# Performance work log

Measured on AMD Instinct MI355X. Metric: run time of the kernel, lower is better.

## Reference

```python
import jax, jax.numpy as jnp
import numpy as np

F, N, D, K = 32, 4096, 64, 512
COMMITMENT_COST = 0.25


def setup_inputs() -> dict:
    key = jax.random.key(0)
    k1, k2 = jax.random.split(key)
    inputs = jax.random.normal(k1, (F, N, D), dtype=jnp.float32)
    # GlorotUniform on weight shape [F, D, K]
    limit = float(np.sqrt(6.0 / (D + K)))
    w = jax.random.uniform(k2, (F, D, K), dtype=jnp.float32, minval=-limit, maxval=limit)
    return {"inputs": inputs, "w": w}


def reference(inputs, w):
    # inputs: [F, N, D], w: [F, D, K]
    distances = (
        jnp.sum(inputs ** 2, axis=2, keepdims=True)
        - 2.0 * jnp.einsum('fnd,fdk->fnk', inputs, w)
        + jnp.sum(w ** 2, axis=1, keepdims=True)
    )
    enc_idx = jnp.argmin(distances, axis=2)  # [F, N]
    w_t = jnp.swapaxes(w, 1, 2)  # [F, K, D]
    quantized = jnp.take_along_axis(w_t, enc_idx[:, :, None], axis=1)  # [F, N, D]
    e_latent_loss = jnp.mean((jax.lax.stop_gradient(quantized) - inputs) ** 2)
    q_latent_loss = jnp.mean((quantized - jax.lax.stop_gradient(inputs)) ** 2)
    loss = q_latent_loss + COMMITMENT_COST * e_latent_loss
    # straight-through estimator
    output = inputs + jax.lax.stop_gradient(quantized - inputs)
    return output, loss
```

## Files before the change

### kernel.cpp

```cpp
#include <hip/hip_runtime.h>
#include <math.h>

#define NF 32
#define NN 4096
#define ND 64
#define NK 512

#define LOSS_SCALE (1.25f / (float)(NF * NN * ND))
#define RESCUE_TAU 5.5e-4f

typedef short bf16x8 __attribute__((ext_vector_type(8)));
typedef float f32x4 __attribute__((ext_vector_type(4)));

static __device__ __forceinline__ unsigned short f2bf_rne(float f) {
    unsigned int u = __float_as_uint(f);
    u += 0x7FFFu + ((u >> 16) & 1u);
    return (unsigned short)(u >> 16);
}
static __device__ __forceinline__ float bf2f(unsigned short h) {
    return __uint_as_float(((unsigned int)h) << 16);
}

static __device__ __forceinline__ void gload_lds16(const void* g, void* l) {
    __builtin_amdgcn_global_load_lds(
        (const __attribute__((address_space(1))) unsigned int*)g,
        (__attribute__((address_space(3))) unsigned int*)l, 16, 0, 0);
}

__global__ __launch_bounds__(256)
void vq_prep_w(const float* __restrict__ w, float* __restrict__ wt,
               unsigned short* __restrict__ wh, unsigned short* __restrict__ wl,
               float* __restrict__ w2h, float* __restrict__ loss_slot) {
    __shared__ float lds[64 * 65];
    const int t  = threadIdx.x;
    const int f  = blockIdx.x >> 3;
    const int k0 = (blockIdx.x & 7) * 64;
    const float* __restrict__ wf = w + (size_t)f * ND * NK;

    if (blockIdx.x == 0 && t == 0) *loss_slot = 0.0f;

    {
        const int d = t >> 2, qq = t & 3;
#pragma unroll
        for (int i = 0; i < 4; ++i) {
            const int c4 = qq + i * 4;
            const float4 v = *(const float4*)(wf + (size_t)d * NK + k0 + c4 * 4);
            lds[d * 65 + c4 * 4 + 0] = v.x;
            lds[d * 65 + c4 * 4 + 1] = v.y;
            lds[d * 65 + c4 * 4 + 2] = v.z;
            lds[d * 65 + c4 * 4 + 3] = v.w;
        }
    }
    __syncthreads();

    const int k = t >> 2, p = t & 3;
    float v[16];
    float s = 0.0f;
#pragma unroll
    for (int j = 0; j < 16; ++j) {
        v[j] = lds[(p * 16 + j) * 65 + k];
        s = fmaf(v[j], v[j], s);
    }
    s += __shfl_xor(s, 1, 64);
    s += __shfl_xor(s, 2, 64);
    if (p == 0) w2h[f * NK + k0 + k] = 0.5f * s;

    const size_t rowo = ((size_t)f * NK + k0 + k) * ND + p * 16;
    unsigned short hh[16], ll[16];
#pragma unroll
    for (int j = 0; j < 16; ++j) {
        hh[j] = f2bf_rne(v[j]);
        ll[j] = f2bf_rne(v[j] - bf2f(hh[j]));
    }
#pragma unroll
    for (int i = 0; i < 4; ++i) {
        *(float4*)(wt + rowo + i * 4) =
            make_float4(v[i*4+0], v[i*4+1], v[i*4+2], v[i*4+3]);
        *(ushort4*)(wh + rowo + i * 4) =
            make_ushort4(hh[i*4+0], hh[i*4+1], hh[i*4+2], hh[i*4+3]);
        *(ushort4*)(wl + rowo + i * 4) =
            make_ushort4(ll[i*4+0], ll[i*4+1], ll[i*4+2], ll[i*4+3]);
    }
}

__global__ __launch_bounds__(256, 4)
void vq_argmin(const float* __restrict__ x_in,
               const unsigned short* __restrict__ wh,
               const unsigned short* __restrict__ wl,
               const float* __restrict__ wt,
               const float* __restrict__ w2h,
               float* __restrict__ out,
               float* __restrict__ loss_slot) {
    const int b    = blockIdx.x;
    const int j    = b >> 3;
    const int f    = (b & 7) * 4 + (j & 3);
    const int xt   = j >> 2;
    const int tid  = threadIdx.x;
    const int wave = tid >> 6;
    const int lane = tid & 63;
    const int lc   = lane & 15;
    const int q    = lane >> 4;
    const int n0   = xt * 128 + wave * 32;
    const int g0b  = f * NN + xt * 128;

    __shared__ float w2s[NK];
    __shared__ __align__(16) unsigned short bstage[2][8192];
    __shared__ unsigned int lds_key[128];
    __shared__ unsigned char lds_flag[128];
    __shared__ float wsum[4];

    for (int t = tid; t < NK; t += 256) w2s[t] = w2h[f * NK + t];

    bf16x8 ah[2][2], al[2][2];
    const float* __restrict__ xbase = x_in + ((size_t)f * NN + n0 + lc) * ND;
#pragma unroll
    for (int mt = 0; mt < 2; ++mt) {
#pragma unroll
        for (int s = 0; s < 2; ++s) {
            const float* p = xbase + mt * 16 * ND + s * 32 + q * 8;
            float4 u0 = *(const float4*)(p);
            float4 u1 = *(const float4*)(p + 4);
            float xv[8] = {-u0.x, -u0.y, -u0.z, -u0.w, -u1.x, -u1.y, -u1.z, -u1.w};
            bf16x8 hh, ll;
#pragma unroll
            for (int jj = 0; jj < 8; ++jj) {
                unsigned short hb = f2bf_rne(xv[jj]);
                unsigned short lb = f2bf_rne(xv[jj] - bf2f(hb));
                hh[jj] = (short)hb;
                ll[jj] = (short)lb;
            }
            ah[mt][s] = hh;
            al[mt][s] = ll;
        }
    }

    const unsigned short* __restrict__ whf = wh + (size_t)f * NK * ND;
    const unsigned short* __restrict__ wlf = wl + (size_t)f * NK * ND;

    float k1[8], k2[8];
#pragma unroll
    for (int ri = 0; ri < 8; ++ri) { k1[ri] = INFINITY; k2[ri] = INFINITY; }

#define STAGE(st, pb) do {                                                  \
    _Pragma("unroll")                                                       \
    for (int rep = 0; rep < 4; ++rep) {                                     \
        const int c  = wave * 4 + rep;                                      \
        const int tl = c >> 2;                                              \
        const int sg = (c >> 1) & 1;                                        \
        const unsigned short* src = ((c & 1) ? wlf : whf) +                 \
            (size_t)((st) * 64 + tl * 16 + lc) * ND + q * 8 + sg * 32;      \
        gload_lds16(src, &bstage[pb][c * 512]);                             \
    }                                                                       \
} while (0)

    STAGE(0, 0);

    for (int st = 0; st < 8; ++st) {
        __syncthreads();
        if (st < 7) STAGE(st + 1, (st + 1) & 1);
        const unsigned short* __restrict__ bb = &bstage[st & 1][0];

#pragma unroll
        for (int tl = 0; tl < 4; ++tl) {
            const int col = st * 64 + tl * 16 + lc;
            bf16x8 bh0 = *(const bf16x8*)(bb + (tl * 4 + 0) * 512 + lane * 8);
            bf16x8 bl0 = *(const bf16x8*)(bb + (tl * 4 + 1) * 512 + lane * 8);
            bf16x8 bh1 = *(const bf16x8*)(bb + (tl * 4 + 2) * 512 + lane * 8);
            bf16x8 bl1 = *(const bf16x8*)(bb + (tl * 4 + 3) * 512 + lane * 8);
            const float w2 = w2s[col];
#pragma unroll
            for (int mt = 0; mt < 2; ++mt) {
                f32x4 c = {w2, w2, w2, w2};
                c = __builtin_amdgcn_mfma_f32_16x16x32_bf16(ah[mt][0], bh0, c, 0, 0, 0);
                c = __builtin_amdgcn_mfma_f32_16x16x32_bf16(ah[mt][1], bh1, c, 0, 0, 0);
                c = __builtin_amdgcn_mfma_f32_16x16x32_bf16(ah[mt][0], bl0, c, 0, 0, 0);
                c = __builtin_amdgcn_mfma_f32_16x16x32_bf16(ah[mt][1], bl1, c, 0, 0, 0);
                c = __builtin_amdgcn_mfma_f32_16x16x32_bf16(al[mt][0], bh0, c, 0, 0, 0);
                c = __builtin_amdgcn_mfma_f32_16x16x32_bf16(al[mt][1], bh1, c, 0, 0, 0);
#pragma unroll
                for (int r = 0; r < 4; ++r) {
                    const int ri = mt * 4 + r;
                    const float key = __uint_as_float(
                        (__float_as_uint(c[r]) & 0xFFFFFE00u) | (unsigned int)col);
                    k2[ri] = __builtin_amdgcn_fmed3f(key, k1[ri], k2[ri]);
                    k1[ri] = fminf(key, k1[ri]);
                }
            }
        }
    }

#pragma unroll
    for (int ri = 0; ri < 8; ++ri) {
        float a1 = k1[ri], a2 = k2[ri];
#pragma unroll
        for (int off = 1; off < 16; off <<= 1) {
            const float b1 = __shfl_xor(a1, off, 64);
            const float b2 = __shfl_xor(a2, off, 64);
            a2 = fminf(fminf(a2, b2), fmaxf(a1, b1));
            a1 = fminf(a1, b1);
        }
        k1[ri] = a1; k2[ri] = a2;
    }

    if (lc == 0) {
#pragma unroll
        for (int mt = 0; mt < 2; ++mt) {
#pragma unroll
            for (int r = 0; r < 4; ++r) {
                const int ri = mt * 4 + r;
                const int lr = wave * 32 + mt * 16 + q * 4 + r;
                const unsigned int u1 = __float_as_uint(k1[ri]);
                const unsigned int u2 = __float_as_uint(k2[ri]);
                lds_key[lr] = u1 & 0x1FFu;
                const float s1 = __uint_as_float(u1 & 0xFFFFFE00u);
                const float s2 = __uint_as_float(u2 & 0xFFFFFE00u);
                lds_flag[lr] = (s2 - s1 < RESCUE_TAU) ? 1 : 0;
            }
        }
    }
    __syncthreads();

    {
        const int lr32 = wave * 32 + (lane & 31);
        const int fl = (lane < 32) ? lds_flag[lr32] : 0;
        unsigned long long mm = __ballot(fl != 0);
        const float* __restrict__ wtf = wt + (size_t)f * NK * ND;
        while (mm) {
            const int r = __ffsll(mm) - 1;
            mm &= mm - 1;
            const int grow = g0b + wave * 32 + r;
            const float* __restrict__ xr = x_in + (size_t)grow * ND;
            unsigned long long best = 0xFFFFFFFFFFFFFFFFULL;
#pragma unroll 1
            for (int jj = 0; jj < 8; ++jj) {
                const int col = jj * 64 + lane;
                const float* __restrict__ wr = wtf + (size_t)col * ND;
                float t = w2s[col];
#pragma unroll
                for (int d = 0; d < ND; d += 4) {
                    float4 xv = *(const float4*)(xr + d);
                    float4 wv = *(const float4*)(wr + d);
                    t = fmaf(-xv.x, wv.x, t);
                    t = fmaf(-xv.y, wv.y, t);
                    t = fmaf(-xv.z, wv.z, t);
                    t = fmaf(-xv.w, wv.w, t);
                }
                unsigned int u = __float_as_uint(t);
                u ^= (unsigned int)((int)u >> 31) | 0x80000000u;
                const unsigned long long key =
                    ((unsigned long long)u << 32) | (unsigned int)col;
                best = key < best ? key : best;
            }
#pragma unroll
            for (int off = 32; off > 0; off >>= 1) {
                const unsigned long long o = __shfl_xor(best, off, 64);
                best = o < best ? o : best;
            }
            if (lane == 0) lds_key[wave * 32 + r] = (unsigned int)(best & 0x1FFu);
        }
    }
    __syncthreads();

    {
        const int row_l = tid >> 1;
        const int part  = tid & 1;
        const int grow  = g0b + row_l;
        const unsigned int k = lds_key[row_l];
        const float* __restrict__ q32 = wt + ((size_t)f * NK + k) * ND + part * 32;
        const float* __restrict__ x32 = x_in + (size_t)grow * ND + part * 32;
        float* __restrict__ o32       = out + (size_t)grow * ND + part * 32;

        float lsum = 0.0f;
#pragma unroll
        for (int jj = 0; jj < 8; ++jj) {
            float4 qv = *(const float4*)(q32 + 4 * jj);
            float4 xv = *(const float4*)(x32 + 4 * jj);
            const float dx0 = qv.x - xv.x;
            const float dx1 = qv.y - xv.y;
            const float dx2 = qv.z - xv.z;
            const float dx3 = qv.w - xv.w;
            lsum = fmaf(dx0, dx0, lsum);
            lsum = fmaf(dx1, dx1, lsum);
            lsum = fmaf(dx2, dx2, lsum);
            lsum = fmaf(dx3, dx3, lsum);
            *(float4*)(o32 + 4 * jj) = qv;
        }

#pragma unroll
        for (int off = 32; off > 0; off >>= 1) {
            lsum += __shfl_down(lsum, off, 64);
        }
        if ((tid & 63) == 0) wsum[tid >> 6] = lsum;
        __syncthreads();
        if (tid == 0) {
            atomicAdd(loss_slot,
                      (wsum[0] + wsum[1] + wsum[2] + wsum[3]) * LOSS_SCALE);
        }
    }
}

extern "C" void kernel_launch(void* const* d_in, const int* in_sizes, int n_in,
                              void* d_out, int out_size, void* d_ws, size_t ws_size,
                              hipStream_t stream) {
    const float* x_in = (const float*)d_in[0];
    const float* w    = (const float*)d_in[1];
    float* out        = (float*)d_out;

    float* wt  = (float*)d_ws;
    float* w2h = wt + (size_t)NF * NK * ND;
    unsigned short* wh = (unsigned short*)(w2h + NF * NK);
    unsigned short* wl = wh + (size_t)NF * NK * ND;

    float* loss_slot = out + (size_t)NF * NN * ND;

    vq_prep_w<<<NF * 8, 256, 0, stream>>>(w, wt, wh, wl, w2h, loss_slot);

    vq_argmin<<<NF * NN / 128, 256, 0, stream>>>(x_in, wh, wl, wt, w2h,
                                                 out, loss_slot);
}
```

Before: 146.0 us.

## Split MFMA accumulator chains and reuse register-held inputs via LDS for loss

New measurement: 155.8 us. 6.7% more time.

```diff
diff --git a/kernel.cpp b/kernel.cpp
--- a/kernel.cpp
+++ b/kernel.cpp
@@ -170,20 +170,49 @@
             const float w2 = w2s[col];
 #pragma unroll
             for (int mt = 0; mt < 2; ++mt) {
-                f32x4 c = {w2, w2, w2, w2};
-                c = __builtin_amdgcn_mfma_f32_16x16x32_bf16(ah[mt][0], bh0, c, 0, 0, 0);
-                c = __builtin_amdgcn_mfma_f32_16x16x32_bf16(ah[mt][1], bh1, c, 0, 0, 0);
-                c = __builtin_amdgcn_mfma_f32_16x16x32_bf16(ah[mt][0], bl0, c, 0, 0, 0);
-                c = __builtin_amdgcn_mfma_f32_16x16x32_bf16(ah[mt][1], bl1, c, 0, 0, 0);
-                c = __builtin_amdgcn_mfma_f32_16x16x32_bf16(al[mt][0], bh0, c, 0, 0, 0);
-                c = __builtin_amdgcn_mfma_f32_16x16x32_bf16(al[mt][1], bh1, c, 0, 0, 0);
+                f32x4 cA = {w2, w2, w2, w2};
+                f32x4 cB = {0.0f, 0.0f, 0.0f, 0.0f};
+                cA = __builtin_amdgcn_mfma_f32_16x16x32_bf16(ah[mt][0], bh0, cA, 0, 0, 0);
+                cB = __builtin_amdgcn_mfma_f32_16x16x32_bf16(ah[mt][1], bh1, cB, 0, 0, 0);
+                cA = __builtin_amdgcn_mfma_f32_16x16x32_bf16(ah[mt][0], bl0, cA, 0, 0, 0);
+                cB = __builtin_amdgcn_mfma_f32_16x16x32_bf16(ah[mt][1], bl1, cB, 0, 0, 0);
+                cA = __builtin_amdgcn_mfma_f32_16x16x32_bf16(al[mt][0], bh0, cA, 0, 0, 0);
+                cB = __builtin_amdgcn_mfma_f32_16x16x32_bf16(al[mt][1], bh1, cB, 0, 0, 0);
 #pragma unroll
                 for (int r = 0; r < 4; ++r) {
                     const int ri = mt * 4 + r;
+                    const float sc = cA[r] + cB[r];
                     const float key = __uint_as_float(
-                        (__float_as_uint(c[r]) & 0xFFFFFE00u) | (unsigned int)col);
+                        (__float_as_uint(sc) & 0xFFFFFE00u) | (unsigned int)col);
                     k2[ri] = __builtin_amdgcn_fmed3f(key, k1[ri], k2[ri]);
                     k1[ri] = fminf(key, k1[ri]);
+                }
+            }
+        }
+    }
+
+    __syncthreads();
+    {
+        float* __restrict__ xs = (float*)&bstage[0][0];
+#pragma unroll
+        for (int mt = 0; mt < 2; ++mt) {
+#pragma unroll
+            for (int s = 0; s < 2; ++s) {
+                const int row = wave * 32 + mt * 16 + lc;
+                const int cc0 = s * 8 + q * 2;
+#pragma unroll
+                for (int t2 = 0; t2 < 2; ++t2) {
+                    const int cc = cc0 + t2;
+                    float4 v;
+                    v.x = -(bf2f((unsigned short)ah[mt][s][t2*4+0]) +
+                            bf2f((unsigned short)al[mt][s][t2*4+0]));
+                    v.y = -(bf2f((unsigned short)ah[mt][s][t2*4+1]) +
+                            bf2f((unsigned short)al[mt][s][t2*4+1]));
+                    v.z = -(bf2f((unsigned short)ah[mt][s][t2*4+2]) +
+                            bf2f((unsigned short)al[mt][s][t2*4+2]));
+                    v.w = -(bf2f((unsigned short)ah[mt][s][t2*4+3]) +
+                            bf2f((unsigned short)al[mt][s][t2*4+3]));
+                    *(float4*)(xs + row * 64 + ((cc ^ (row & 15)) << 2)) = v;
                 }
             }
         }
@@ -267,14 +296,15 @@
         const int grow  = g0b + row_l;
         const unsigned int k = lds_key[row_l];
         const float* __restrict__ q32 = wt + ((size_t)f * NK + k) * ND + part * 32;
-        const float* __restrict__ x32 = x_in + (size_t)grow * ND + part * 32;
+        const float* __restrict__ xs  = (const float*)&bstage[0][0];
         float* __restrict__ o32       = out + (size_t)grow * ND + part * 32;
 
         float lsum = 0.0f;
 #pragma unroll
         for (int jj = 0; jj < 8; ++jj) {
+            const int cc = part * 8 + jj;
             float4 qv = *(const float4*)(q32 + 4 * jj);
-            float4 xv = *(const float4*)(x32 + 4 * jj);
+            float4 xv = *(const float4*)(xs + row_l * 64 + ((cc ^ (row_l & 15)) << 2));
             const float dx0 = qv.x - xv.x;
             const float dx1 = qv.y - xv.y;
             const float dx2 = qv.z - xv.z;
```
